# Kernel tuning notes

Measured on AMD Instinct MI355X. Metric: run time of the kernel, lower is better.

Reference implementation:

```python
import jax, jax.numpy as jnp
import numpy as np
from jax import lax

# QKeras quantized_bits(8, 0, alpha=1, keep_negative=1):
#   delta = 2^-(bits-1) = 1/128, q(x) = clip(round(x*128), -128, 127)/128
QB_SCALE = 128.0
# QKeras quantized_relu(8, 0): q(x) = clip(round(x*256), 0, 255)/256
QR_SCALE = 256.0

def _ste(q, x):
    # straight-through estimator: forward = q(x), backward = identity
    return x + lax.stop_gradient(q - x)

def qbits(x):
    q = jnp.clip(jnp.round(x * QB_SCALE), -QB_SCALE, QB_SCALE - 1.0) / QB_SCALE
    return _ste(q, x)

def qrelu(x):
    q = jnp.clip(jnp.round(x * QR_SCALE), 0.0, QR_SCALE - 1.0) / QR_SCALE
    return _ste(q, x)


def setup_inputs() -> dict:
    key = jax.random.key(0)
    ks = jax.random.split(key, 9)
    B, C, F = 1000000, 16, 3
    dims = [C * F, 64, 32, 32]
    x = jax.random.normal(ks[0], (B, C, F), dtype=jnp.float32)
    def w(k, i, o):
        return jax.random.normal(k, (i, o), dtype=jnp.float32) * (0.5 / np.sqrt(i))
    inp = {"x": x}
    for li in range(3):
        inp[f"w{li+1}"] = w(ks[1 + 2 * li], dims[li], dims[li + 1])
        inp[f"b{li+1}"] = jax.random.normal(ks[2 + 2 * li], (dims[li + 1],), dtype=jnp.float32) * 0.05
    inp["wout"] = w(ks[7], dims[-1], 5)
    inp["bout"] = jax.random.normal(ks[8], (5,), dtype=jnp.float32) * 0.05
    return inp


def reference(x, w1, b1, w2, b2, w3, b3, wout, bout):
    h = x.reshape(x.shape[0], -1)  # Flatten: [B, 48]
    for w, b in ((w1, b1), (w2, b2), (w3, b3)):
        # QDense: fake-quantize kernel & bias, fp32 matmul, quantized_relu
        h = qrelu(h @ qbits(w) + qbits(b))
    return h @ wout + bout  # final float Dense -> logits [B, 5]
```

## Files before the change

### kernel.cpp

```cpp
#include <hip/hip_runtime.h>

typedef short  short8 __attribute__((ext_vector_type(8)));
typedef float  f32x4  __attribute__((ext_vector_type(4)));
typedef unsigned int u32;
typedef unsigned long long u64;
typedef unsigned short u16;

__device__ __forceinline__ u32 f2bf(float v) {
    u32 u = __float_as_uint(v);
    return (u + 0x7FFFu + ((u >> 16) & 1u)) >> 16;
}
__device__ __forceinline__ float qround128(float w) {
    float q = rintf(w * 128.0f);
    return fminf(fmaxf(q, -128.0f), 127.0f);
}
__device__ __forceinline__ u64 qrelu_pack4(f32x4 a) {
    u32 u0 = __float_as_uint(fminf(fmaxf(rintf(a[0]), 0.f), 255.f));
    u32 u1 = __float_as_uint(fminf(fmaxf(rintf(a[1]), 0.f), 255.f));
    u32 u2 = __float_as_uint(fminf(fmaxf(rintf(a[2]), 0.f), 255.f));
    u32 u3 = __float_as_uint(fminf(fmaxf(rintf(a[3]), 0.f), 255.f));
    u32 lo = (u0 >> 16) | (u1 & 0xFFFF0000u);
    u32 hi = (u2 >> 16) | (u3 & 0xFFFF0000u);
    return (u64)lo | ((u64)hi << 32);
}
union FragU { short8 s; u32 u[4]; };
__device__ __forceinline__ f32x4 mfma16(short8 a, short8 b, f32x4 c) {
    return __builtin_amdgcn_mfma_f32_16x16x32_bf16(a, b, c, 0, 0, 0);
}


__global__ void prep(const float* __restrict__ w1, const float* __restrict__ b1,
                     const float* __restrict__ w2, const float* __restrict__ b2,
                     const float* __restrict__ w3, const float* __restrict__ b3,
                     const float* __restrict__ wo, const float* __restrict__ bo,
                     u16* __restrict__ wsh) {
    int t = threadIdx.x;
    for (int idx = t; idx < 16 * 512; idx += 256) {
        int blk = idx >> 9, e = idx & 511;
        int l = e >> 3, j = e & 7;
        int r  = l & 15;
        int kk = ((l >> 4) << 3) + j;
        float val = 0.f;
        if (blk < 8) {
            int mt = blk >> 1, ks = blk & 1;
            int k = ks * 32 + kk, fo = mt * 16 + r;
            if (k < 48) val = 2.0f * qround128(w1[k * 64 + fo]);
        } else if (blk < 12) {
            int bi = blk - 8, mt = bi >> 1, ks = bi & 1;
            int k = ks * 32 + kk, fo = mt * 16 + r;
            val = qround128(w2[k * 32 + fo]) * (1.0f / 128.0f);
        } else if (blk < 14) {
            int mt = blk - 12;
            val = qround128(w3[kk * 32 + mt * 16 + r]) * (1.0f / 128.0f);
        } else {
            float wv = (r < 5) ? wo[kk * 5 + r] * (1.0f / 256.0f) : 0.f;
            u32 hb = f2bf(wv);
            if (blk == 14) { wsh[idx] = (u16)hb; continue; }
            val = wv - __uint_as_float(hb << 16);
        }
        wsh[idx] = (u16)f2bf(val);
    }
    float* wsf = (float*)(wsh + 8192);
    for (int i = t; i < 64; i += 256) wsf[i]       = 2.0f * qround128(b1[i]);
    for (int i = t; i < 32; i += 256) wsf[64 + i]  = 2.0f * qround128(b2[i]);
    for (int i = t; i < 32; i += 256) wsf[96 + i]  = 2.0f * qround128(b3[i]);
    for (int i = t; i < 16; i += 256) wsf[128 + i] = (i < 5) ? bo[i] : 0.f;
}


__global__ __launch_bounds__(256) void mlp_mfma(const float* __restrict__ x,
                                                const u16* __restrict__ wsh,
                                                float* __restrict__ out, int ntiles) {
    __shared__ __align__(16) u16 smem[4][3840];
    const int tid = threadIdx.x;
    const int wid = tid >> 6, lane = tid & 63;
    const int c = lane & 15, g = lane >> 4;

    short8 wf[16];
    const short8* wv = (const short8*)wsh;
    #pragma unroll
    for (int i = 0; i < 16; ++i) wf[i] = wv[i * 64 + lane];

    const float* wsf = (const float*)(wsh + 8192);
    f32x4 b1q[4], b2q[2], b3q[2], boq;
    #pragma unroll
    for (int i = 0; i < 4; ++i) b1q[i] = *(const f32x4*)(wsf + i * 16 + 4 * g);
    #pragma unroll
    for (int i = 0; i < 2; ++i) b2q[i] = *(const f32x4*)(wsf + 64 + i * 16 + 4 * g);
    #pragma unroll
    for (int i = 0; i < 2; ++i) b3q[i] = *(const f32x4*)(wsf + 96 + i * 16 + 4 * g);
    boq = *(const f32x4*)(wsf + 128 + 4 * g);

    u16* H = &smem[wid][0];

    const int gw = blockIdx.x * 4 + wid;
    const int nw = gridDim.x * 4;

    for (int t0 = gw; t0 < ntiles; t0 += nw) {
        const float* xl = x + (size_t)t0 * 768 + (c * 48 + g * 8);
        float4 xa = *(const float4*)(xl);
        float4 xb = *(const float4*)(xl + 4);
        float4 xc = {0.f, 0.f, 0.f, 0.f}, xd = {0.f, 0.f, 0.f, 0.f};
        if (g < 2) { xc = *(const float4*)(xl + 32); xd = *(const float4*)(xl + 36); }

        float v0[8] = {xa.x, xa.y, xa.z, xa.w, xb.x, xb.y, xb.z, xb.w};
        float v1[8] = {xc.x, xc.y, xc.z, xc.w, xd.x, xd.y, xd.z, xd.w};
        FragU bh0, bl0, bh1, bl1;
        #pragma unroll
        for (int p = 0; p < 4; ++p) {
            u32 a0 = f2bf(v0[2 * p]), a1 = f2bf(v0[2 * p + 1]);
            float r0 = v0[2 * p] - __uint_as_float(a0 << 16);
            float r1 = v0[2 * p + 1] - __uint_as_float(a1 << 16);
            bh0.u[p] = a0 | (a1 << 16);
            bl0.u[p] = f2bf(r0) | (f2bf(r1) << 16);
            u32 c0 = f2bf(v1[2 * p]), c1 = f2bf(v1[2 * p + 1]);
            float s0 = v1[2 * p] - __uint_as_float(c0 << 16);
            float s1 = v1[2 * p + 1] - __uint_as_float(c1 << 16);
            bh1.u[p] = c0 | (c1 << 16);
            bl1.u[p] = f2bf(s0) | (f2bf(s1) << 16);
        }

        #pragma unroll
        for (int mt = 0; mt < 4; ++mt) {
            f32x4 a = b1q[mt];
            a = mfma16(wf[mt * 2 + 0], bh0.s, a);
            a = mfma16(wf[mt * 2 + 1], bh1.s, a);
            a = mfma16(wf[mt * 2 + 0], bl0.s, a);
            a = mfma16(wf[mt * 2 + 1], bl1.s, a);
            *(u64*)(H + c * 80 + mt * 16 + 4 * g) = qrelu_pack4(a);
        }

        short8 p0 = *(const short8*)(H + c * 80 + 8 * g);
        short8 p1 = *(const short8*)(H + c * 80 + 32 + 8 * g);
        #pragma unroll
        for (int mt = 0; mt < 2; ++mt) {
            f32x4 a = b2q[mt];
            a = mfma16(wf[8 + mt * 2 + 0], p0, a);
            a = mfma16(wf[8 + mt * 2 + 1], p1, a);
            *(u64*)(H + 1280 + c * 80 + mt * 16 + 4 * g) = qrelu_pack4(a);
        }

        short8 p2 = *(const short8*)(H + 1280 + c * 80 + 8 * g);
        #pragma unroll
        for (int mt = 0; mt < 2; ++mt) {
            f32x4 a = b3q[mt];
            a = mfma16(wf[12 + mt], p2, a);
            *(u64*)(H + 2560 + c * 80 + mt * 16 + 4 * g) = qrelu_pack4(a);
        }

        short8 p3 = *(const short8*)(H + 2560 + c * 80 + 8 * g);
        f32x4 ao = boq;
        ao = mfma16(wf[14], p3, ao);
        ao = mfma16(wf[15], p3, ao);

        float* orow = out + (size_t)t0 * 80 + c * 5;
        if (g == 0) {
            orow[0] = ao[0]; orow[1] = ao[1]; orow[2] = ao[2]; orow[3] = ao[3];
        } else if (g == 1) {
            orow[4] = ao[0];
        }
    }
}

extern "C" void kernel_launch(void* const* d_in, const int* in_sizes, int n_in,
                              void* d_out, int out_size, void* d_ws, size_t ws_size,
                              hipStream_t stream) {
    const float* x  = (const float*)d_in[0];
    const float* w1 = (const float*)d_in[1];
    const float* b1 = (const float*)d_in[2];
    const float* w2 = (const float*)d_in[3];
    const float* b2 = (const float*)d_in[4];
    const float* w3 = (const float*)d_in[5];
    const float* b3 = (const float*)d_in[6];
    const float* wo = (const float*)d_in[7];
    const float* bo = (const float*)d_in[8];
    float* out = (float*)d_out;

    int B = in_sizes[0] / 48;
    int ntiles = B / 16;

    prep<<<1, 256, 0, stream>>>(w1, b1, w2, b2, w3, b3, wo, bo, (u16*)d_ws);

    int blocks = (ntiles + 3) / 4;
    if (blocks > 2048) blocks = 2048;
    mlp_mfma<<<blocks, 256, 0, stream>>>(x, (const u16*)d_ws, out, ntiles);
}
```

Before: 61.02 us.

## Prefetch next tile's inputs, use packed bf16 conversion, raise occupancy hint

Software-pipelines the x loads by fetching the next tile's inputs into registers while the current tile runs through the MLP, so global load latency is hidden behind MFMA work. It also replaces the manual bit-twiddling bf16 rounding with the packed float2-to-bfloat162 conversion intrinsic, which may map to a single hardware convert instruction. The launch bounds now request 2 blocks per CU, which constrains register use. Together these target memory latency stalls and ALU overhead in the split-bf16 input conversion, at the cost of extra registers for the prefetch buffers and possible spills under the tighter register budget.

Measured after the change: 60.39 us. Within noise of the previous version (-1.0%).

```diff
diff --git a/kernel.cpp b/kernel.cpp
--- a/kernel.cpp
+++ b/kernel.cpp
@@ -1,4 +1,5 @@
 #include <hip/hip_runtime.h>
+#include <hip/hip_bf16.h>
 
 typedef short  short8 __attribute__((ext_vector_type(8)));
 typedef float  f32x4  __attribute__((ext_vector_type(4)));
@@ -14,14 +15,16 @@
     float q = rintf(w * 128.0f);
     return fminf(fmaxf(q, -128.0f), 127.0f);
 }
+__device__ __forceinline__ u32 cvtpk(float a, float b) {
+    __hip_bfloat162 h = __float22bfloat162_rn(make_float2(a, b));
+    union { __hip_bfloat162 h; u32 u; } cv; cv.h = h; return cv.u;
+}
 __device__ __forceinline__ u64 qrelu_pack4(f32x4 a) {
-    u32 u0 = __float_as_uint(fminf(fmaxf(rintf(a[0]), 0.f), 255.f));
-    u32 u1 = __float_as_uint(fminf(fmaxf(rintf(a[1]), 0.f), 255.f));
-    u32 u2 = __float_as_uint(fminf(fmaxf(rintf(a[2]), 0.f), 255.f));
-    u32 u3 = __float_as_uint(fminf(fmaxf(rintf(a[3]), 0.f), 255.f));
-    u32 lo = (u0 >> 16) | (u1 & 0xFFFF0000u);
-    u32 hi = (u2 >> 16) | (u3 & 0xFFFF0000u);
-    return (u64)lo | ((u64)hi << 32);
+    float q0 = fminf(fmaxf(rintf(a[0]), 0.f), 255.f);
+    float q1 = fminf(fmaxf(rintf(a[1]), 0.f), 255.f);
+    float q2 = fminf(fmaxf(rintf(a[2]), 0.f), 255.f);
+    float q3 = fminf(fmaxf(rintf(a[3]), 0.f), 255.f);
+    return (u64)cvtpk(q0, q1) | ((u64)cvtpk(q2, q3) << 32);
 }
 union FragU { short8 s; u32 u[4]; };
 __device__ __forceinline__ f32x4 mfma16(short8 a, short8 b, f32x4 c) {
@@ -68,9 +71,9 @@
 }
 
 
-__global__ __launch_bounds__(256) void mlp_mfma(const float* __restrict__ x,
-                                                const u16* __restrict__ wsh,
-                                                float* __restrict__ out, int ntiles) {
+__global__ __launch_bounds__(256, 2) void mlp_mfma(const float* __restrict__ x,
+                                                   const u16* __restrict__ wsh,
+                                                   float* __restrict__ out, int ntiles) {
     __shared__ __align__(16) u16 smem[4][3840];
     const int tid = threadIdx.x;
     const int wid = tid >> 6, lane = tid & 63;
@@ -92,32 +95,43 @@
     boq = *(const f32x4*)(wsf + 128 + 4 * g);
 
     u16* H = &smem[wid][0];
+    const int xoff = c * 48 + g * 8;
 
     const int gw = blockIdx.x * 4 + wid;
     const int nw = gridDim.x * 4;
 
+    const float* xl = x + (size_t)gw * 768 + xoff;
+    float4 xa = *(const float4*)(xl);
+    float4 xb = *(const float4*)(xl + 4);
+    float4 xc = {0.f, 0.f, 0.f, 0.f}, xd = {0.f, 0.f, 0.f, 0.f};
+    if (g < 2) { xc = *(const float4*)(xl + 32); xd = *(const float4*)(xl + 36); }
+
     for (int t0 = gw; t0 < ntiles; t0 += nw) {
-        const float* xl = x + (size_t)t0 * 768 + (c * 48 + g * 8);
-        float4 xa = *(const float4*)(xl);
-        float4 xb = *(const float4*)(xl + 4);
-        float4 xc = {0.f, 0.f, 0.f, 0.f}, xd = {0.f, 0.f, 0.f, 0.f};
-        if (g < 2) { xc = *(const float4*)(xl + 32); xd = *(const float4*)(xl + 36); }
+        const int t1 = t0 + nw;
+        const bool have = t1 < ntiles;
+        float4 na, nb, nc, nd;
+        if (have) {
+            const float* nl = x + (size_t)t1 * 768 + xoff;
+            na = *(const float4*)(nl);
+            nb = *(const float4*)(nl + 4);
+            if (g < 2) { nc = *(const float4*)(nl + 32); nd = *(const float4*)(nl + 36); }
+        }
 
         float v0[8] = {xa.x, xa.y, xa.z, xa.w, xb.x, xb.y, xb.z, xb.w};
         float v1[8] = {xc.x, xc.y, xc.z, xc.w, xd.x, xd.y, xd.z, xd.w};
         FragU bh0, bl0, bh1, bl1;
         #pragma unroll
         for (int p = 0; p < 4; ++p) {
-            u32 a0 = f2bf(v0[2 * p]), a1 = f2bf(v0[2 * p + 1]);
-            float r0 = v0[2 * p] - __uint_as_float(a0 << 16);
-            float r1 = v0[2 * p + 1] - __uint_as_float(a1 << 16);
-            bh0.u[p] = a0 | (a1 << 16);
-            bl0.u[p] = f2bf(r0) | (f2bf(r1) << 16);
-            u32 c0 = f2bf(v1[2 * p]), c1 = f2bf(v1[2 * p + 1]);
-            float s0 = v1[2 * p] - __uint_as_float(c0 << 16);
-            float s1 = v1[2 * p + 1] - __uint_as_float(c1 << 16);
-            bh1.u[p] = c0 | (c1 << 16);
-            bl1.u[p] = f2bf(s0) | (f2bf(s1) << 16);
+            u32 u = cvtpk(v0[2 * p], v0[2 * p + 1]);
+            bh0.u[p] = u;
+            float r0 = v0[2 * p]     - __uint_as_float(u << 16);
+            float r1 = v0[2 * p + 1] - __uint_as_float(u & 0xFFFF0000u);
+            bl0.u[p] = cvtpk(r0, r1);
+            u32 w = cvtpk(v1[2 * p], v1[2 * p + 1]);
+            bh1.u[p] = w;
+            float s0 = v1[2 * p]     - __uint_as_float(w << 16);
+            float s1 = v1[2 * p + 1] - __uint_as_float(w & 0xFFFF0000u);
+            bl1.u[p] = cvtpk(s0, s1);
         }
 
         #pragma unroll
@@ -159,6 +173,8 @@
         } else if (g == 1) {
             orow[4] = ao[0];
         }
+
+        if (have) { xa = na; xb = nb; if (g < 2) { xc = nc; xd = nd; } }
     }
 }
 
```
